# Kernel tuning notes

Hardware: AMD Instinct MI355X
Metric: run time of the kernel (lower is better)

## Reference

```python
import jax, jax.numpy as jnp
import numpy as np

N = 65536   # batch_size * timeseries
D = 512     # feature dim of h_real
K = 64      # n_clusters


def setup_inputs() -> dict:
    key = jax.random.key(0)
    k1, k2 = jax.random.split(key)
    h_real = jax.random.normal(k1, (N, D), dtype=jnp.float32)
    # F is an (approximately) orthogonal projection parameter [N, K].
    F = jax.random.normal(k2, (N, K), dtype=jnp.float32)
    return {"h_real": h_real, "F": F}


def reference(h_real, F):
    # Original: WTW = h h^T (N x N); loss = trace(WTW) - trace(F^T WTW F).
    # Algebraically identical reduced form, never materializing the N x N Gram:
    #   trace(h h^T) = sum(h * h)
    #   trace(F^T h h^T F) = ||F^T h||_F^2
    tr_wtw = jnp.sum(h_real * h_real)
    G = F.T @ h_real                      # [K, D] skinny GEMM
    tr_proj = jnp.sum(G * G)
    return tr_wtw - tr_proj
```

## Files before the change

### kernel.cpp

```cpp
#include <hip/hip_runtime.h>
#include <hip/hip_fp16.h>
#include <hip/hip_bf16.h>

#define N_TOT 65536
#define D_DIM 512
#define K_DIM 64
#define NC    32
#define GSZ   (K_DIM * D_DIM)
#define NBLK  512

typedef __bf16   bf16x8 __attribute__((ext_vector_type(8)));
typedef float    f32x4  __attribute__((ext_vector_type(4)));
typedef _Float16 half8  __attribute__((ext_vector_type(8)));

union pk4 { unsigned int u[4]; bf16x8 v; };

__device__ __forceinline__ unsigned int pack2(float a, float b) {
    __hip_bfloat162 t = __float22bfloat162_rn(make_float2(a, b));
    union { __hip_bfloat162 h; unsigned int u; } r; r.h = t;
    return r.u;
}

typedef __attribute__((address_space(3))) void       lds_void;
typedef __attribute__((address_space(1))) const void gbl_void;

__device__ __forceinline__ void dma16(const float* g, float* l) {
    __builtin_amdgcn_global_load_lds((gbl_void*)g, (lds_void*)l, 16, 0, 0);
}

extern "C" __global__ void __launch_bounds__(512, 4)
k1_partial(const float* __restrict__ h, const float* __restrict__ F,
           float* __restrict__ trw_out, unsigned short* __restrict__ gpart,
           float* __restrict__ out, int rowsPerBlock) {
    __shared__ float hbuf[NC][D_DIM];
    __shared__ float fbuf[NC][K_DIM];
    __shared__ float red[8];

    const int tid = threadIdx.x;
    const int b   = blockIdx.x;
    if (b == 0 && tid == 0) out[0] = 0.0f;

    const int wave = tid >> 6;
    const int lane = tid & 63;
    const int m    = lane & 15;
    const int q    = lane >> 4;

    const int row0    = b * rowsPerBlock;
    const int nChunks = rowsPerBlock / NC;

    f32x4 acc[4][4];
    #pragma unroll
    for (int kt = 0; kt < 4; ++kt)
        #pragma unroll
        for (int dt = 0; dt < 4; ++dt)
            acc[kt][dt] = (f32x4){0.f, 0.f, 0.f, 0.f};

    float trw = 0.f;

    for (int c = 0; c < nChunks; ++c) {
        const int r0 = row0 + c * NC;
        {
            const float* g = h + (size_t)(r0 + 4 * wave) * D_DIM + lane * 4;
            #pragma unroll
            for (int rr = 0; rr < 4; ++rr)
                #pragma unroll
                for (int hf = 0; hf < 2; ++hf)
                    dma16(g + rr * D_DIM + hf * 256, &hbuf[4 * wave + rr][hf * 256]);
            const float* gf = F + (size_t)(r0 + 4 * wave) * K_DIM + lane * 4;
            dma16(gf, &fbuf[4 * wave][0]);
        }
        __syncthreads();

        bf16x8 bfrag[4], afrag[4];
        #pragma unroll
        for (int dt = 0; dt < 4; ++dt) {
            float v[8];
            #pragma unroll
            for (int j = 0; j < 8; ++j) {
                v[j] = hbuf[q * 8 + j][wave * 64 + dt * 16 + m];
                trw += v[j] * v[j];
            }
            pk4 pp;
            #pragma unroll
            for (int jj = 0; jj < 4; ++jj) pp.u[jj] = pack2(v[2*jj], v[2*jj+1]);
            bfrag[dt] = pp.v;
        }
        #pragma unroll
        for (int kt = 0; kt < 4; ++kt) {
            float v[8];
            #pragma unroll
            for (int j = 0; j < 8; ++j)
                v[j] = fbuf[q * 8 + j][kt * 16 + m];
            pk4 pp;
            #pragma unroll
            for (int jj = 0; jj < 4; ++jj) pp.u[jj] = pack2(v[2*jj], v[2*jj+1]);
            afrag[kt] = pp.v;
        }
        #pragma unroll
        for (int kt = 0; kt < 4; ++kt)
            #pragma unroll
            for (int dt = 0; dt < 4; ++dt)
                acc[kt][dt] = __builtin_amdgcn_mfma_f32_16x16x32_bf16(
                    afrag[kt], bfrag[dt], acc[kt][dt], 0, 0, 0);

        __syncthreads();
    }

    unsigned short* gp = gpart + (size_t)b * GSZ;
    #pragma unroll
    for (int kt = 0; kt < 4; ++kt)
        #pragma unroll
        for (int dt = 0; dt < 4; ++dt)
            #pragma unroll
            for (int r = 0; r < 4; ++r) {
                const int k = kt * 16 + q * 4 + r;
                const int d = wave * 64 + dt * 16 + m;
                __half hv = __float2half(acc[kt][dt][r]);
                gp[k * D_DIM + d] = *(unsigned short*)&hv;
            }

    #pragma unroll
    for (int off = 32; off > 0; off >>= 1) trw += __shfl_down(trw, off, 64);
    if (lane == 0) red[wave] = trw;
    __syncthreads();
    if (tid == 0) {
        float s = 0.f;
        #pragma unroll
        for (int w = 0; w < 8; ++w) s += red[w];
        trw_out[b] = s;
    }
}

extern "C" __global__ void __launch_bounds__(512)
k2_reduce(const float* __restrict__ trw, const unsigned short* __restrict__ gpart,
          float* __restrict__ out, int P) {
    __shared__ float sh[32 * 16 * 8];
    __shared__ float red2[8];

    const int tid = threadIdx.x;
    const int sub = tid >> 4;
    const int oct = tid & 15;
    const int tt  = blockIdx.x * 16 + oct;

    float g[8];
    #pragma unroll
    for (int j = 0; j < 8; ++j) g[j] = 0.f;

    const unsigned short* base = gpart + (size_t)tt * 8;
    for (int b = sub; b < P; b += 32) {
        half8 v = *(const half8*)(base + (size_t)b * GSZ);
        #pragma unroll
        for (int j = 0; j < 8; ++j) g[j] += (float)v[j];
    }
    #pragma unroll
    for (int j = 0; j < 8; ++j) sh[(sub * 16 + oct) * 8 + j] = g[j];
    __syncthreads();

    float val = 0.f;
    if (tid < 128) {
        const int o2 = tid >> 3, j = tid & 7;
        float s = 0.f;
        #pragma unroll
        for (int sb = 0; sb < 32; ++sb) s += sh[(sb * 16 + o2) * 8 + j];
        val = -s * s;
    } else if (blockIdx.x == 0) {
        for (int i = tid - 128; i < P; i += 384)
            val += trw[i];
    }

    #pragma unroll
    for (int off = 32; off > 0; off >>= 1) val += __shfl_down(val, off, 64);
    if ((tid & 63) == 0) red2[tid >> 6] = val;
    __syncthreads();
    if (tid == 0) {
        float s = 0.f;
        #pragma unroll
        for (int w = 0; w < 8; ++w) s += red2[w];
        atomicAdd(out, s);
    }
}

extern "C" void kernel_launch(void* const* d_in, const int* in_sizes, int n_in,
                              void* d_out, int out_size, void* d_ws, size_t ws_size,
                              hipStream_t stream) {
    const float* h = (const float*)d_in[0];
    const float* F = (const float*)d_in[1];
    float* out = (float*)d_out;

    int P = NBLK;
    while (P > 1 && (size_t)4096 + (size_t)P * (GSZ * 2) > ws_size) P >>= 1;
    const int rowsPerBlock = N_TOT / P;

    float* trw = (float*)d_ws;
    unsigned short* gpart = (unsigned short*)((char*)d_ws + 4096);

    hipLaunchKernelGGL(k1_partial, dim3(P), dim3(512), 0, stream,
                       h, F, trw, gpart, out, rowsPerBlock);
    hipLaunchKernelGGL(k2_reduce, dim3(256), dim3(512), 0, stream,
                       trw, gpart, out, P);
}
```

Baseline: 216.4 us.

## Load h and F directly into registers and split D across two blocks

Removes the LDS staging (global_load_lds DMA plus barriers) and has each lane load its MFMA operand elements straight from global memory into registers. The grid becomes 1024 blocks of 256 threads, each covering 128 rows and half of D. Blocks of the same slab write disjoint halves of one fp16 partial. The trace partials grow to 1024 entries. Per-lane global loads are strided (16 consecutive floats across lanes per row), so coalescing is worse than the 16-byte DMA. The workspace-size fallback for the partial count is dropped.

New measurement: 214.6 us. About the same (-0.8%).

```diff
diff --git a/kernel.cpp b/kernel.cpp
--- a/kernel.cpp
+++ b/kernel.cpp
@@ -5,9 +5,9 @@
 #define N_TOT 65536
 #define D_DIM 512
 #define K_DIM 64
+#define SLABS 512
 #define NC    32
 #define GSZ   (K_DIM * D_DIM)
-#define NBLK  512
 
 typedef __bf16   bf16x8 __attribute__((ext_vector_type(8)));
 typedef float    f32x4  __attribute__((ext_vector_type(4)));
@@ -21,32 +21,25 @@
     return r.u;
 }
 
-typedef __attribute__((address_space(3))) void       lds_void;
-typedef __attribute__((address_space(1))) const void gbl_void;
-
-__device__ __forceinline__ void dma16(const float* g, float* l) {
-    __builtin_amdgcn_global_load_lds((gbl_void*)g, (lds_void*)l, 16, 0, 0);
-}
-
-extern "C" __global__ void __launch_bounds__(512, 4)
+extern "C" __global__ void __launch_bounds__(256, 1)
 k1_partial(const float* __restrict__ h, const float* __restrict__ F,
            float* __restrict__ trw_out, unsigned short* __restrict__ gpart,
-           float* __restrict__ out, int rowsPerBlock) {
-    __shared__ float hbuf[NC][D_DIM];
-    __shared__ float fbuf[NC][K_DIM];
-    __shared__ float red[8];
+           float* __restrict__ out) {
+    __shared__ float red[4];
 
-    const int tid = threadIdx.x;
-    const int b   = blockIdx.x;
-    if (b == 0 && tid == 0) out[0] = 0.0f;
+    const int tid   = threadIdx.x;
+    const int bx    = blockIdx.x;
+    const int slab  = bx >> 1;
+    const int dhalf = bx & 1;
+    if (bx == 0 && tid == 0) out[0] = 0.0f;
 
     const int wave = tid >> 6;
     const int lane = tid & 63;
     const int m    = lane & 15;
     const int q    = lane >> 4;
+    const int d0   = dhalf * 256 + wave * 64;
 
-    const int row0    = b * rowsPerBlock;
-    const int nChunks = rowsPerBlock / NC;
+    const int n0 = slab * 128;
 
     f32x4 acc[4][4];
     #pragma unroll
@@ -57,56 +50,52 @@
 
     float trw = 0.f;
 
-    for (int c = 0; c < nChunks; ++c) {
-        const int r0 = row0 + c * NC;
-        {
-            const float* g = h + (size_t)(r0 + 4 * wave) * D_DIM + lane * 4;
+    for (int c = 0; c < 4; ++c) {
+        const float* hb = h + (size_t)(n0 + c * NC + q * 8) * D_DIM + d0 + m;
+        const float* fb = F + (size_t)(n0 + c * NC + q * 8) * K_DIM + m;
+
+        float vb[32], va[32];
+        #pragma unroll
+        for (int dt = 0; dt < 4; ++dt)
             #pragma unroll
-            for (int rr = 0; rr < 4; ++rr)
-                #pragma unroll
-                for (int hf = 0; hf < 2; ++hf)
-                    dma16(g + rr * D_DIM + hf * 256, &hbuf[4 * wave + rr][hf * 256]);
-            const float* gf = F + (size_t)(r0 + 4 * wave) * K_DIM + lane * 4;
-            dma16(gf, &fbuf[4 * wave][0]);
-        }
-        __syncthreads();
+            for (int j = 0; j < 8; ++j)
+                vb[dt * 8 + j] = hb[(size_t)j * D_DIM + dt * 16];
+        #pragma unroll
+        for (int kt = 0; kt < 4; ++kt)
+            #pragma unroll
+            for (int j = 0; j < 8; ++j)
+                va[kt * 8 + j] = fb[(size_t)j * K_DIM + kt * 16];
 
         bf16x8 bfrag[4], afrag[4];
         #pragma unroll
         for (int dt = 0; dt < 4; ++dt) {
-            float v[8];
-            #pragma unroll
-            for (int j = 0; j < 8; ++j) {
-                v[j] = hbuf[q * 8 + j][wave * 64 + dt * 16 + m];
-                trw += v[j] * v[j];
-            }
             pk4 pp;
             #pragma unroll
-            for (int jj = 0; jj < 4; ++jj) pp.u[jj] = pack2(v[2*jj], v[2*jj+1]);
+            for (int jj = 0; jj < 4; ++jj) {
+                float a0 = vb[dt * 8 + 2 * jj], a1 = vb[dt * 8 + 2 * jj + 1];
+                trw += a0 * a0 + a1 * a1;
+                pp.u[jj] = pack2(a0, a1);
+            }
             bfrag[dt] = pp.v;
         }
         #pragma unroll
         for (int kt = 0; kt < 4; ++kt) {
-            float v[8];
-            #pragma unroll
-            for (int j = 0; j < 8; ++j)
-                v[j] = fbuf[q * 8 + j][kt * 16 + m];
             pk4 pp;
             #pragma unroll
-            for (int jj = 0; jj < 4; ++jj) pp.u[jj] = pack2(v[2*jj], v[2*jj+1]);
+            for (int jj = 0; jj < 4; ++jj)
+                pp.u[jj] = pack2(va[kt * 8 + 2 * jj], va[kt * 8 + 2 * jj + 1]);
             afrag[kt] = pp.v;
         }
+
         #pragma unroll
         for (int kt = 0; kt < 4; ++kt)
             #pragma unroll
             for (int dt = 0; dt < 4; ++dt)
                 acc[kt][dt] = __builtin_amdgcn_mfma_f32_16x16x32_bf16(
                     afrag[kt], bfrag[dt], acc[kt][dt], 0, 0, 0);
-
-        __syncthreads();
     }
 
-    unsigned short* gp = gpart + (size_t)b * GSZ;
+    unsigned short* gp = gpart + (size_t)slab * GSZ;
     #pragma unroll
     for (int kt = 0; kt < 4; ++kt)
         #pragma unroll
@@ -114,7 +103,7 @@
             #pragma unroll
             for (int r = 0; r < 4; ++r) {
                 const int k = kt * 16 + q * 4 + r;
-                const int d = wave * 64 + dt * 16 + m;
+                const int d = d0 + dt * 16 + m;
                 __half hv = __float2half(acc[kt][dt][r]);
                 gp[k * D_DIM + d] = *(unsigned short*)&hv;
             }
@@ -123,17 +112,13 @@
     for (int off = 32; off > 0; off >>= 1) trw += __shfl_down(trw, off, 64);
     if (lane == 0) red[wave] = trw;
     __syncthreads();
-    if (tid == 0) {
-        float s = 0.f;
-        #pragma unroll
-        for (int w = 0; w < 8; ++w) s += red[w];
-        trw_out[b] = s;
-    }
+    if (tid == 0)
+        trw_out[bx] = red[0] + red[1] + red[2] + red[3];
 }
 
 extern "C" __global__ void __launch_bounds__(512)
 k2_reduce(const float* __restrict__ trw, const unsigned short* __restrict__ gpart,
-          float* __restrict__ out, int P) {
+          float* __restrict__ out, int Pg, int Pt) {
     __shared__ float sh[32 * 16 * 8];
     __shared__ float red2[8];
 
@@ -147,8 +132,8 @@
     for (int j = 0; j < 8; ++j) g[j] = 0.f;
 
     const unsigned short* base = gpart + (size_t)tt * 8;
-    for (int b = sub; b < P; b += 32) {
-        half8 v = *(const half8*)(base + (size_t)b * GSZ);
+    for (int s = sub; s < Pg; s += 32) {
+        half8 v = *(const half8*)(base + (size_t)s * GSZ);
         #pragma unroll
         for (int j = 0; j < 8; ++j) g[j] += (float)v[j];
     }
@@ -164,7 +149,7 @@
         for (int sb = 0; sb < 32; ++sb) s += sh[(sb * 16 + o2) * 8 + j];
         val = -s * s;
     } else if (blockIdx.x == 0) {
-        for (int i = tid - 128; i < P; i += 384)
+        for (int i = tid - 128; i < Pt; i += 384)
             val += trw[i];
     }
 
@@ -187,15 +172,11 @@
     const float* F = (const float*)d_in[1];
     float* out = (float*)d_out;
 
-    int P = NBLK;
-    while (P > 1 && (size_t)4096 + (size_t)P * (GSZ * 2) > ws_size) P >>= 1;
-    const int rowsPerBlock = N_TOT / P;
-
     float* trw = (float*)d_ws;
     unsigned short* gpart = (unsigned short*)((char*)d_ws + 4096);
 
-    hipLaunchKernelGGL(k1_partial, dim3(P), dim3(512), 0, stream,
-                       h, F, trw, gpart, out, rowsPerBlock);
+    hipLaunchKernelGGL(k1_partial, dim3(SLABS * 2), dim3(256), 0, stream,
+                       h, F, trw, gpart, out);
     hipLaunchKernelGGL(k2_reduce, dim3(256), dim3(512), 0, stream,
-                       trw, gpart, out, P);
+                       trw, gpart, out, SLABS, SLABS * 2);
 }
```
